# Kernel optimization log

Hardware: AMD Instinct MI355X
Metric: run time of the kernel (lower is better)

Reference implementation:

```python
import jax, jax.numpy as jnp
import numpy as np

H = 128; R = 8; VN = 100; VA = 64
N = 8192; B = 64; L = 48; E = 65536


def setup_inputs() -> dict:
    key = jax.random.key(0)
    ks = jax.random.split(key, 24)
    s = 0.05
    nodeTypes = jax.random.randint(ks[0], (N,), 0, VN)
    edge_index = jax.random.randint(ks[1], (2, E), 0, N)
    edge_attr = jax.random.randint(ks[2], (E,), 0, R)
    bs = jnp.repeat(jnp.arange(B), N // B)              # sorted node->graph map
    nodes_bs = jnp.full((B,), N // B, dtype=jnp.int32)  # nodes per graph
    len_seq = jax.random.randint(ks[3], (B,), 1, L + 1).at[0].set(L)  # max == L
    sequence_input = (jax.random.uniform(ks[4], (N, L)) < 0.05).astype(jnp.float32)
    action_input = jax.random.randint(ks[5], (B,), 0, VA)
    params = dict(
        emb_nodes=jax.random.normal(ks[6], (VN, H)) * s,
        emb_actions=jax.random.normal(ks[7], (VA, H)) * s,
        rgcn_rel=jax.random.normal(ks[8], (3, R, H, H)) * s,   # per-layer relation weights
        rgcn_root=jax.random.normal(ks[9], (3, H, H)) * s,
        rgcn_bias=jnp.zeros((3, H)),
        gru_w_ih=jax.random.normal(ks[10], (3 * H, H)) * s,
        gru_w_hh=jax.random.normal(ks[11], (3 * H, H)) * s,
        gru_b_ih=jnp.zeros((3 * H,)),
        gru_b_hh=jnp.zeros((3 * H,)),
        linA_w=jax.random.normal(ks[12], (H, H)) * s,
        linA_b=jnp.zeros((H,)),
        linAf_w=jax.random.normal(ks[13], (VA, H)) * s,
        linAf_b=jnp.zeros((VA,)),
        linN_w=jax.random.normal(ks[14], (H, 2 * H)) * s,
        linN_b=jnp.zeros((H,)),
        linNf_w=jax.random.normal(ks[15], (1, H)) * s,
        linNf_b=jnp.zeros((1,)),
    )
    return dict(nodeTypes=nodeTypes, edge_index=edge_index, edge_attr=edge_attr,
                bs=bs, nodes_bs=nodes_bs, len_seq=len_seq,
                sequence_input=sequence_input, action_input=action_input, **params)


def reference(nodeTypes, edge_index, edge_attr, bs, nodes_bs, len_seq,
              sequence_input, action_input,
              emb_nodes, emb_actions, rgcn_rel, rgcn_root, rgcn_bias,
              gru_w_ih, gru_w_hh, gru_b_ih, gru_b_hh,
              linA_w, linA_b, linAf_w, linAf_b,
              linN_w, linN_b, linNf_w, linNf_b):
    n = nodeTypes.shape[0]
    b = nodes_bs.shape[0]
    h = emb_nodes.shape[1]
    r = rgcn_rel.shape[1]
    l = sequence_input.shape[1]

    x = emb_nodes[nodeTypes]                               # [N,H]
    src, dst = edge_index[0], edge_index[1]
    seg = dst * r + edge_attr                              # per (target, relation) segment
    cnt = jax.ops.segment_sum(jnp.ones((src.shape[0],), x.dtype), seg, n * r)
    denom = jnp.maximum(cnt, 1.0).reshape(n, r, 1)
    for li in range(3):
        agg = jax.ops.segment_sum(x[src], seg, n * r).reshape(n, r, h) / denom
        x = jax.nn.relu(jnp.einsum('nrh,rho->no', agg, rgcn_rel[li])
                        + x @ rgcn_root[li] + rgcn_bias[li])

    # global mean pool -> graph embedding
    h_G = jax.ops.segment_sum(x, bs, b) / nodes_bs[:, None].astype(x.dtype)  # [B,H]
    action = jax.nn.relu(h_G @ linA_w.T + linA_b) @ linAf_w.T + linAf_b      # [B,VA]

    sos = emb_actions[action_input][:, None, :]            # [B,1,H]
    # sequence embeddings: sum over nodes in each graph of seq[i,t]*x[i]
    emb_seq = sequence_input[:, :, None] * x[:, None, :]   # [N,L,H]
    out = jax.ops.segment_sum(emb_seq, bs, b)              # [B,L,H]
    input_gru = jnp.concatenate([sos, out], axis=1)[:, :l] # packed GRU only sees first L steps

    # single-layer GRU, h0 = h_G (torch gate order r,z,n)
    xW = input_gru @ gru_w_ih.T + gru_b_ih                 # [B,L,3H]
    def step(hprev, xw):
        hW = hprev @ gru_w_hh.T + gru_b_hh
        xr, xz, xn = jnp.split(xw, 3, -1)
        hr, hz, hn = jnp.split(hW, 3, -1)
        rg = jax.nn.sigmoid(xr + hr)
        zg = jax.nn.sigmoid(xz + hz)
        ng = jnp.tanh(xn + rg * hn)
        hnew = (1.0 - zg) * ng + zg * hprev
        return hnew, hnew
    _, hs = jax.lax.scan(step, h_G, jnp.swapaxes(xW, 0, 1))
    seq_out = jnp.swapaxes(hs, 0, 1)                       # [B,L,H]
    mask = jnp.arange(l)[None, :] < len_seq[:, None]       # pad_packed zero-pads
    seq_out = seq_out * mask[:, :, None]

    out_gru = seq_out[bs]                                  # repeat_interleave -> [N,L,H]
    concats = jnp.concatenate(
        [out_gru, jnp.broadcast_to(x[:, None, :], (n, l, h))], axis=2)  # [N,L,2H]
    hid = jax.nn.relu(concats @ linN_w.T + linN_b)         # [N,L,H]
    logits = (hid @ linNf_w.T + linNf_b)[..., 0]           # [N,L]

    # scatter_softmax over nodes grouped by graph (dim 0)
    m = jax.lax.stop_gradient(jax.ops.segment_max(logits, bs, b))
    e = jnp.exp(logits - m[bs])
    ssum = jax.ops.segment_sum(e, bs, b)
    nodes_final = e / ssum[bs]
    return action, nodes_final
```

## Files before the change

### kernel.cpp

```cpp
#include <hip/hip_runtime.h>
#include <hip/hip_bf16.h>

#define H   128
#define RR  8
#define NN  8192
#define BB  64
#define LL  48
#define EE  65536
#define NPG 128
#define VA  64
#define NSEG (NN*RR)
#define GPB 16

typedef unsigned short u16;
typedef unsigned int   u32;

__device__ __forceinline__ float b2f(u16 u) {
    union { u32 i; float f; } v; v.i = ((u32)u) << 16; return v.f;
}
__device__ __forceinline__ u16 f2b(float f) {
    union { float f; u32 i; } v; v.f = f;
    u32 x = v.i;
    return (u16)((x + 0x7fffu + ((x >> 16) & 1u)) >> 16);
}
__device__ __forceinline__ float2 up2(u32 p) {
    union { u32 i; float f; } a, b;
    a.i = p << 16; b.i = p & 0xffff0000u;
    return make_float2(a.f, b.f);
}
__device__ __forceinline__ u32 pk2(float a, float b) {
    return ((u32)f2b(b) << 16) | (u32)f2b(a);
}
__device__ __forceinline__ float rcpf(float x) { return __builtin_amdgcn_rcpf(x); }
__device__ __forceinline__ u32 cvtpk(float lo, float hi) {
    u32 r;
    asm("v_cvt_pk_bf16_f32 %0, %1, %2" : "=v"(r) : "v"(lo), "v"(hi));
    return r;
}

#define K_LOG2E  1.4426950408889634f
#define K_2LOG2E 2.8853900817779268f

typedef __attribute__((ext_vector_type(8))) short bf16x8;
typedef __attribute__((ext_vector_type(4))) float f32x4;
typedef __attribute__((ext_vector_type(4))) unsigned short u16x4;

__global__ __launch_bounds__(256) void k_prep(const int* __restrict__ nodeTypes,
                                              const float* __restrict__ emb_nodes,
                                              const float* __restrict__ rel,
                                              const float* __restrict__ root,
                                              const float* __restrict__ w_ih,
                                              float* __restrict__ x0,
                                              u16* __restrict__ WTt,
                                              u16* __restrict__ WTih,
                                              float* __restrict__ hGsum,
                                              int* __restrict__ fill) {
    int idx = blockIdx.x * 256 + threadIdx.x;
    if (idx < NSEG) fill[idx] = 0;
    if (idx < 384 * H) WTih[idx] = f2b(w_ih[idx]);
    if (idx < BB * H) hGsum[idx] = 0.f;
    if (idx < NN * H) {
        int n = idx >> 7, h = idx & (H - 1);
        x0[idx] = emb_nodes[(size_t)nodeTypes[n] * H + h];
    }
    int j = idx - NN * H;
    if (j < 0 || j >= 3 * 147456) return;
    int li  = j / 147456;
    int rem = j - li * 147456;
    int tile = rem / 36864;
    int r2   = rem - tile * 36864;
    int ks   = r2 / 1024;
    int r3   = r2 - ks * 1024;
    int sub  = r3 >> 9;
    int r4   = r3 & 511;
    int lane = r4 >> 3, jj = r4 & 7;
    int col = tile * 32 + sub * 16 + (lane & 15);
    int k   = ks * 32 + (lane >> 4) * 8 + jj;
    float v;
    if (k < 1024) v = rel[(((size_t)li * RR + (k >> 7)) * H + (k & 127)) * H + col];
    else          v = root[((size_t)li * H + (k - 1024)) * H + col];
    WTt[j] = f2b(v);
}

__global__ __launch_bounds__(256) void k_hist(const int* __restrict__ edge_index,
                                              const int* __restrict__ edge_attr,
                                              int* __restrict__ fill) {
    int e = blockIdx.x * 256 + threadIdx.x;
    if (e < EE) {
        int seg = edge_index[EE + e] * RR + edge_attr[e];
        atomicAdd(&fill[seg], 1);
    }
}

__global__ __launch_bounds__(256) void k_scan1(const int* __restrict__ fill,
                                               int* __restrict__ bsum) {
    __shared__ int red[4];
    int tid = threadIdx.x, lane = tid & 63, wv = tid >> 6;
    int v = fill[blockIdx.x * 256 + tid];
#pragma unroll
    for (int off = 32; off >= 1; off >>= 1) v += __shfl_down(v, off, 64);
    if (lane == 0) red[wv] = v;
    __syncthreads();
    if (tid == 0) bsum[blockIdx.x] = red[0] + red[1] + red[2] + red[3];
}

__global__ __launch_bounds__(256) void k_scan2(const int* __restrict__ bsum,
                                               int* __restrict__ boff,
                                               int* __restrict__ rowptr) {
    __shared__ int s[256];
    int tid = threadIdx.x;
    int v0 = bsum[tid];
    s[tid] = v0;
    __syncthreads();
    for (int off = 1; off < 256; off <<= 1) {
        int v = (tid >= off) ? s[tid - off] : 0;
        __syncthreads();
        s[tid] += v;
        __syncthreads();
    }
    boff[tid] = s[tid] - v0;
    if (tid == 255) rowptr[NSEG] = s[255];
}

__global__ __launch_bounds__(256) void k_scan3(const int* __restrict__ boff,
                                               int* __restrict__ fill,
                                               int* __restrict__ rowptr) {
    __shared__ int s[256];
    int tid = threadIdx.x;
    int g = blockIdx.x * 256 + tid;
    int c = fill[g];
    s[tid] = c;
    __syncthreads();
    for (int off = 1; off < 256; off <<= 1) {
        int v = (tid >= off) ? s[tid - off] : 0;
        __syncthreads();
        s[tid] += v;
        __syncthreads();
    }
    int r = boff[blockIdx.x] + s[tid] - c;
    rowptr[g] = r;
    fill[g] = r;
}

__global__ __launch_bounds__(256) void k_scatter(const int* __restrict__ edge_index,
                                                 const int* __restrict__ edge_attr,
                                                 int* __restrict__ fill,
                                                 int* __restrict__ colidx) {
    int e = blockIdx.x * 256 + threadIdx.x;
    if (e < EE) {
        int seg = edge_index[EE + e] * RR + edge_attr[e];
        int pos = atomicAdd(&fill[seg], 1);
        colidx[pos] = edge_index[e];
    }
}

#define RGN 16
#define EPRE 512

__global__ __launch_bounds__(512) void k_rgcn(const float* __restrict__ xin,
                                              float* __restrict__ xout,
                                              const u16* __restrict__ WTt,
                                              const float* __restrict__ bias,
                                              const int* __restrict__ rowptr,
                                              const int* __restrict__ colidx,
                                              float* __restrict__ hGsum) {
    __shared__ u32 ab[RGN * 580];
    __shared__ int begs[RGN * RR + 1];
    __shared__ int eidx[EPRE];
    int tid = threadIdx.x, wv = tid >> 6, lane = tid & 63;
    int n0 = blockIdx.x * RGN, segbase = n0 * RR;

    if (tid <= RGN * RR) begs[tid] = rowptr[segbase + tid];
    __syncthreads();
    int E0 = begs[0], ne = begs[RGN * RR] - E0;
    for (int i = tid; i < ne && i < EPRE; i += 512) eidx[i] = colidx[E0 + i];
    __syncthreads();

    for (int s = wv; s < RGN * RR; s += 8) {
        int beg = begs[s], end = begs[s + 1];
        float a0 = 0.f, a1 = 0.f;
        for (int e = beg; e < end; ++e) {
            int off = e - E0;
            int src = (off < EPRE) ? eidx[off] : colidx[e];
            float2 v = ((const float2*)(xin + (size_t)src * H))[lane];
            a0 += v.x; a1 += v.y;
        }
        float inv = 1.f / fmaxf((float)(end - beg), 1.f);
        ab[(s >> 3) * 580 + ((s & 7) << 6) + lane] = pk2(a0 * inv, a1 * inv);
    }
    for (int i = wv; i < RGN; i += 8) {
        const float* xr = xin + (size_t)(n0 + i) * H + 2 * lane;
        ab[i * 580 + 512 + lane] = pk2(xr[0], xr[1]);
    }
    __syncthreads();

    int m = lane & 15, quad = lane >> 4;
    const u32* aP = ab + m * 580 + quad * 4;
    const u32* bT = (const u32*)WTt + (size_t)(wv >> 1) * 36 * 512 + (wv & 1) * 256 + lane * 4;
    f32x4 acc0 = {0.f, 0.f, 0.f, 0.f};
    bf16x8 b0c = *(const bf16x8*)bT;
    for (int ks = 0; ks < 36; ++ks) {
        bf16x8 b0n;
        if (ks < 35) b0n = *(const bf16x8*)(bT + (ks + 1) * 512);
        bf16x8 a = *(const bf16x8*)(aP + ks * 16);
        acc0 = __builtin_amdgcn_mfma_f32_16x16x32_bf16(a, b0c, acc0, 0, 0, 0);
        b0c = b0n;
    }
    int c0 = wv * 16 + m;
    float bv0 = bias[c0];
    float so0 = 0.f;
#pragma unroll
    for (int rg = 0; rg < 4; ++rg) {
        int n = n0 + quad * 4 + rg;
        float o0 = fmaxf(acc0[rg] + bv0, 0.f);
        xout[(size_t)n * H + c0] = o0;
        so0 += o0;
    }
    if (hGsum) {
        so0 += __shfl_xor(so0, 16, 64);
        so0 += __shfl_xor(so0, 32, 64);
        if (quad == 0) {
            int g = n0 >> 7;
            atomicAdd(&hGsum[g * H + c0], so0);
        }
    }
}

__global__ __launch_bounds__(256) void k_pool_seq(const float* __restrict__ hGsum,
                                                  const int* __restrict__ nodes_bs,
                                                  const float* __restrict__ linA_w,
                                                  const float* __restrict__ linA_b,
                                                  const float* __restrict__ linAf_w,
                                                  const float* __restrict__ linAf_b,
                                                  float* __restrict__ hG,
                                                  float* __restrict__ out,
                                                  const float* __restrict__ xf,
                                                  const float* __restrict__ seq,
                                                  const float* __restrict__ emb_actions,
                                                  const int* __restrict__ action_input,
                                                  float* __restrict__ igG) {
    __shared__ float xg[64][H];
    __shared__ u16 lists[LL][64];
    __shared__ int cnts[LL];
    int tid = threadIdx.x;

    if (blockIdx.x < BB) {
        float* hgs = &xg[0][0];
        float* t1  = &xg[1][0];
        int b = blockIdx.x, h = tid;
        if (h < H) {
            float hg = hGsum[(size_t)b * H + h] / (float)nodes_bs[b];
            hG[(size_t)b * H + h] = hg;
            hgs[h] = hg;
        }
        __syncthreads();
        if (h < H) {
            float acc = linA_b[h];
            const float* wr = linA_w + (size_t)h * H;
            for (int k = 0; k < H; ++k) acc += wr[k] * hgs[k];
            t1[h] = fmaxf(acc, 0.f);
        }
        __syncthreads();
        if (h < VA) {
            float a = linAf_b[h];
            const float* w2 = linAf_w + (size_t)h * H;
            for (int k = 0; k < H; ++k) a += w2[k] * t1[k];
            out[(size_t)b * VA + h] = a;
        }
        return;
    }

    int b = blockIdx.x - BB;
    int col = tid & 127, tg = tid >> 7;
    float acc[24];
#pragma unroll
    for (int m = 0; m < 24; ++m) acc[m] = 0.f;

    for (int chunk = 0; chunk < 2; ++chunk) {
        int i0 = b * NPG + chunk * 64;
        __syncthreads();
        if (tid < LL) cnts[tid] = 0;
        __syncthreads();
        for (int idx = tid; idx < 64 * H / 4; idx += 256)
            ((float4*)&xg[0][0])[idx] = ((const float4*)(xf + (size_t)i0 * H))[idx];
        for (int idx = tid; idx < 64 * LL; idx += 256) {
            int i = idx / LL, t = idx - i * LL;
            if (seq[(size_t)(i0 + i) * LL + t] != 0.f) {
                int p = atomicAdd(&cnts[t], 1);
                lists[t][p] = (u16)i;
            }
        }
        __syncthreads();
        for (int m = 0; m < 24; ++m) {
            int t = tg + 2 * m;
            int c = cnts[t];
            float a = acc[m];
            for (int p = 0; p < c; ++p) a += xg[lists[t][p]][col];
            acc[m] = a;
        }
    }
    if (tid < H)
        igG[((size_t)b * LL) * H + tid] = emb_actions[(size_t)action_input[b] * H + tid];
#pragma unroll
    for (int m = 0; m < 24; ++m) {
        int t = tg + 2 * m;
        if (t < LL - 1)
            igG[((size_t)b * LL + t + 1) * H + col] = acc[m];
    }
}

__global__ __launch_bounds__(256) void k_xw(const float* __restrict__ igG,
                                            const u16* __restrict__ WTih,
                                            const float* __restrict__ b_ih,
                                            const float* __restrict__ b_hh,
                                            u16* __restrict__ xwG) {
    __shared__ u32 ab[16 * 68];
    int tid = threadIdx.x, wv = tid >> 6, lane = tid & 63;
    int n0 = blockIdx.x * 16;
    for (int s = tid; s < 16 * 64; s += 256) {
        int row = s >> 6, kp = s & 63;
        float2 v = *(const float2*)(igG + (size_t)(n0 + row) * H + 2 * kp);
        ab[row * 68 + kp] = pk2(v.x, v.y);
    }
    __syncthreads();
    int m = lane & 15, quad = lane >> 4;
    const u32* aP = ab + m * 68 + quad * 4;
    f32x4 acc[6];
#pragma unroll
    for (int i = 0; i < 6; ++i) acc[i] = (f32x4){0.f, 0.f, 0.f, 0.f};
#pragma unroll
    for (int ks = 0; ks < 4; ++ks) {
        bf16x8 a = *(const bf16x8*)(aP + ks * 16);
#pragma unroll
        for (int tc = 0; tc < 6; ++tc) {
            int colr = wv * 96 + tc * 16 + m;
            bf16x8 bfr = *(const bf16x8*)((const u32*)WTih + (size_t)colr * 64 + quad * 4 + ks * 16);
            acc[tc] = __builtin_amdgcn_mfma_f32_16x16x32_bf16(a, bfr, acc[tc], 0, 0, 0);
        }
    }
#pragma unroll
    for (int tc = 0; tc < 6; ++tc) {
        int c = wv * 96 + tc * 16 + m;
        float bv = b_ih[c] + ((c < 256) ? b_hh[c] : 0.f);
        float sc = (c < 256) ? K_LOG2E : K_2LOG2E;
        int R = c & 127, gate = c >> 7;
#pragma unroll
        for (int rg = 0; rg < 4; ++rg) {
            int r = n0 + quad * 4 + rg;
            int bb = r / 48, tt = r - bb * 48;
            size_t o = (((((size_t)(bb >> 4) * LL + tt) * 8 + (R >> 4)) * 3 + gate) * 256)
                     + (((R >> 2) & 3) << 6) + ((bb & 15) << 2) + (R & 3);
            xwG[o] = f2b((acc[tc][rg] + bv) * sc);
        }
    }
}

#define GRU_BLKS 4
#define BX_BLKS  (NN / 32)
#define SMEM_BYTES 33024

__global__ __launch_bounds__(512) void k_gru_bx(const u16* __restrict__ xw2,
                                                const float* __restrict__ hG,
                                                const float* __restrict__ w_hh,
                                                const float* __restrict__ b_hh,
                                                const int* __restrict__ len_seq,
                                                float* __restrict__ soutG,
                                                const float* __restrict__ xf,
                                                const float* __restrict__ linN_w,
                                                const float* __restrict__ linN_b,
                                                u16* __restrict__ BxU) {
    __shared__ __align__(16) char smem[SMEM_BYTES];
    int tid = threadIdx.x;

    if (blockIdx.x >= GRU_BLKS) {
        float* xl = (float*)smem;
        float* wb = (float*)(smem + 16384);
        int bid = blockIdx.x - GRU_BLKS;
        int n0 = bid * 32;
        for (int idx = tid; idx < 32 * H; idx += 512)
            xl[idx] = xf[(size_t)n0 * H + idx];
        int col = tid & 127, g = tid >> 7;
        float bv = linN_b[col];
        float acc[8] = {bv, bv, bv, bv, bv, bv, bv, bv};
        for (int c = 0; c < 4; ++c) {
            int k0 = c * 32;
            __syncthreads();
            for (int idx = tid; idx < 32 * H; idx += 512) {
                int r = idx >> 5, kk = idx & 31;
                wb[kk * 130 + r] = linN_w[(size_t)r * (2 * H) + H + k0 + kk];
            }
            __syncthreads();
#pragma unroll
            for (int kk = 0; kk < 32; ++kk) {
                float w = wb[kk * 130 + col];
#pragma unroll
                for (int j = 0; j < 8; ++j) acc[j] += xl[(g * 8 + j) * H + k0 + kk] * w;
            }
        }
#pragma unroll
        for (int j = 0; j < 8; ++j)
            BxU[(size_t)(n0 + g * 8 + j) * H + col] = f2b(acc[j]);
        return;
    }

    u16* hA = (u16*)smem;
    int lane = tid & 63, wv = tid >> 6;
    int mi = lane & 15, quad = lane >> 4;
    int gblk = blockIdx.x;
    int g_abs = gblk * GPB + mi;
    int R0 = 16 * wv + 4 * quad;

    int eW = (((wv >> 1) * 64) + (mi + 16 * ((2 * wv + (quad >> 1)) & 3))) * 8
             + 4 * (quad & 1);

    bf16x8 wfr[3][4];
#pragma unroll
    for (int gate = 0; gate < 3; ++gate) {
        int T = wv + 8 * gate;
        float sc = (gate == 2) ? K_2LOG2E : K_LOG2E;
#pragma unroll
        for (int ks = 0; ks < 4; ++ks) {
            const float* wp = w_hh + (size_t)(16 * T + mi) * H + quad * 8 + ks * 32;
            float4 f0 = *(const float4*)wp;
            float4 f1 = *(const float4*)(wp + 4);
            bf16x8 v;
            v[0] = (short)f2b(f0.x * sc); v[1] = (short)f2b(f0.y * sc);
            v[2] = (short)f2b(f0.z * sc); v[3] = (short)f2b(f0.w * sc);
            v[4] = (short)f2b(f1.x * sc); v[5] = (short)f2b(f1.y * sc);
            v[6] = (short)f2b(f1.z * sc); v[7] = (short)f2b(f1.w * sc);
            wfr[gate][ks] = v;
        }
    }
    float4 bn = *(const float4*)(b_hh + 256 + R0);
    float4 h0 = *(const float4*)(hG + (size_t)g_abs * H + R0);
    int ls = len_seq[g_abs];

    float hp[4]  = {h0.x, h0.y, h0.z, h0.w};
    float bnn[4] = {bn.x * K_2LOG2E, bn.y * K_2LOG2E, bn.z * K_2LOG2E, bn.w * K_2LOG2E};

    auto storeh = [&](int buf, const float* hv) {
        u32 w0 = cvtpk(hv[0], hv[1]);
        u32 w1 = cvtpk(hv[2], hv[3]);
        float2 e0 = up2(w0), e1 = up2(w1);
        u32 l0 = cvtpk(hv[0] - e0.x, hv[1] - e0.y);
        u32 l1 = cvtpk(hv[2] - e1.x, hv[3] - e1.y);
        *(uint2*)&hA[buf * 4096 + eW]        = make_uint2(w0, w1);
        *(uint2*)&hA[buf * 4096 + 2048 + eW] = make_uint2(l0, l1);
    };
    auto loadxw = [&](int t, u16x4* d) {
        const u16* p = xw2 + ((((size_t)gblk * LL + t) * 8 + wv) * 3) * 256
                     + (quad << 6) + (mi << 2);
        d[0] = *(const u16x4*)(p);
        d[1] = *(const u16x4*)(p + 256);
        d[2] = *(const u16x4*)(p + 512);
    };

    auto step = [&](int t, const u16x4* x, int buf) {
        f32x4 acc[3];
        acc[0] = (f32x4){0.f, 0.f, 0.f, 0.f};
        acc[1] = (f32x4){0.f, 0.f, 0.f, 0.f};
        acc[2] = (f32x4){bnn[0], bnn[1], bnn[2], bnn[3]};
#pragma unroll
        for (int ks = 0; ks < 4; ++ks) {
            const int e = (ks * 64 + lane) * 8;
            bf16x8 bh = *(const bf16x8*)&hA[buf * 4096 + e];
            bf16x8 bl = *(const bf16x8*)&hA[buf * 4096 + 2048 + e];
#pragma unroll
            for (int gate = 0; gate < 3; ++gate) {
                acc[gate] = __builtin_amdgcn_mfma_f32_16x16x32_bf16(wfr[gate][ks], bh, acc[gate], 0, 0, 0);
                acc[gate] = __builtin_amdgcn_mfma_f32_16x16x32_bf16(wfr[gate][ks], bl, acc[gate], 0, 0, 0);
            }
        }
        float hv[4];
        float4 so;
#pragma unroll
        for (int r = 0; r < 4; ++r) {
            float xr = b2f(x[0][r]);
            float xz = b2f(x[1][r]);
            float xn = b2f(x[2][r]);
            float rg = rcpf(1.f + __builtin_amdgcn_exp2f(-(xr + acc[0][r])));
            float zg = rcpf(1.f + __builtin_amdgcn_exp2f(-(xz + acc[1][r])));
            float u  = xn + rg * acc[2][r];
            float ng = 1.f - 2.f * rcpf(__builtin_amdgcn_exp2f(u) + 1.f);
            float hn = ng + zg * (hp[r] - ng);
            hp[r] = hn;
            hv[r] = hn;
            ((float*)&so)[r] = (t < ls) ? hn : 0.f;
        }
        *(float4*)(soutG + ((size_t)g_abs * LL + t) * H + R0) = so;
        storeh(buf ^ 1, hv);
    };

    u16x4 xa[3], xb[3];
    loadxw(0, xa);
    loadxw(1, xb);
    storeh(0, hp);
    asm volatile("s_waitcnt lgkmcnt(0)\n\ts_barrier" ::: "memory");

    for (int t = 0; t < LL; t += 2) {
        step(t, xa, 0);
        if (t + 2 < LL) loadxw(t + 2, xa);
        asm volatile("s_waitcnt lgkmcnt(0)\n\ts_barrier" ::: "memory");
        step(t + 1, xb, 1);
        if (t + 3 < LL) loadxw(t + 3, xb);
        asm volatile("s_waitcnt lgkmcnt(0)\n\ts_barrier" ::: "memory");
    }
}

__global__ __launch_bounds__(256) void k_a2(const float* __restrict__ soutG,
                                            const float* __restrict__ linN_w,
                                            float* __restrict__ A2) {
    __shared__ float wb[32][130];
    __shared__ float xl[16][H];
    int tid = threadIdx.x;
    int n0 = blockIdx.x * 16;
    for (int idx = tid; idx < 16 * H; idx += 256)
        xl[idx >> 7][idx & 127] = soutG[(size_t)n0 * H + idx];
    int col = tid & 127, g = tid >> 7;
    float acc[8] = {0.f, 0.f, 0.f, 0.f, 0.f, 0.f, 0.f, 0.f};
    for (int c = 0; c < 4; ++c) {
        int k0 = c * 32;
        __syncthreads();
        for (int idx = tid; idx < 32 * H; idx += 256) {
            int r = idx >> 5, kk = idx & 31;
            wb[kk][r] = linN_w[(size_t)r * (2 * H) + k0 + kk];
        }
        __syncthreads();
#pragma unroll
        for (int kk = 0; kk < 32; ++kk) {
            float w = wb[kk][col];
#pragma unroll
            for (int j = 0; j < 8; ++j) acc[j] += xl[g * 8 + j][k0 + kk] * w;
        }
    }
#pragma unroll
    for (int j = 0; j < 8; ++j)
        A2[(size_t)(n0 + g * 8 + j) * H + col] = acc[j];
}

__global__ __launch_bounds__(256) void k_logits(const float* __restrict__ A2,
                                                const u16* __restrict__ BxU,
                                                const float* __restrict__ linNf_w,
                                                float* __restrict__ logits) {
    __shared__ float a2s[LL][130];
    __shared__ float bxs[16][130];
    __shared__ float w2s[H];
    int tid = threadIdx.x;
    int g = blockIdx.x >> 3, tile = blockIdx.x & 7;
    int n0g = g * NPG + tile * 16;

    for (int i2 = tid; i2 < LL * 64; i2 += 256) {
        int r = i2 >> 6, c2 = i2 & 63;
        *(float2*)&a2s[r][2 * c2] = *(const float2*)(A2 + ((size_t)g * LL + r) * H + 2 * c2);
    }
    for (int iu = tid; iu < 16 * 64; iu += 256) {
        int r = iu >> 6, c = iu & 63;
        float2 v = up2(((const u32*)BxU)[(size_t)(n0g + r) * 64 + c]);
        *(float2*)&bxs[r][2 * c] = v;
    }
    if (tid < H) w2s[tid] = linNf_w[tid];
    __syncthreads();

    int n = tid & 15, tt = tid >> 4;
#pragma unroll
    for (int pass = 0; pass < 3; ++pass) {
        int t = tt + 16 * pass;
        float acc = 0.f;
#pragma unroll
        for (int kp = 0; kp < 64; ++kp) {
            float2 a2 = *(const float2*)&a2s[t][2 * kp];
            float2 bx = *(const float2*)&bxs[n][2 * kp];
            float2 w  = *(const float2*)&w2s[2 * kp];
            acc += w.x * fmaxf(a2.x + bx.x, 0.f) + w.y * fmaxf(a2.y + bx.y, 0.f);
        }
        logits[(size_t)(n0g + n) * LL + t] = acc;
    }
}

__global__ __launch_bounds__(256) void k_softmax(const float* __restrict__ logits,
                                                 float* __restrict__ out) {
    __shared__ float lg[NPG][LL + 1];
    __shared__ float pm[4][LL], ps[4][LL];
    __shared__ float mv[LL], inv[LL];
    int b = blockIdx.x, tid = threadIdx.x;
    int n0 = b * NPG;
    for (int idx = tid; idx < NPG * LL; idx += 256) {
        int n = idx / LL, t = idx - n * LL;
        lg[n][t] = logits[(size_t)n0 * LL + idx];
    }
    __syncthreads();
    int t = tid & 63, seg = tid >> 6;
    if (t < LL) {
        float m = -1e30f;
        int nb = seg * 32;
        for (int n = nb; n < nb + 32; ++n) m = fmaxf(m, lg[n][t]);
        pm[seg][t] = m;
    }
    __syncthreads();
    if (tid < LL)
        mv[tid] = fmaxf(fmaxf(pm[0][tid], pm[1][tid]), fmaxf(pm[2][tid], pm[3][tid]));
    __syncthreads();
    if (t < LL) {
        float m = mv[t], s = 0.f;
        int nb = seg * 32;
        for (int n = nb; n < nb + 32; ++n) {
            float e = __expf(lg[n][t] - m);
            lg[n][t] = e;
            s += e;
        }
        ps[seg][t] = s;
    }
    __syncthreads();
    if (tid < LL)
        inv[tid] = 1.f / (ps[0][tid] + ps[1][tid] + ps[2][tid] + ps[3][tid]);
    __syncthreads();
    for (int idx = tid; idx < NPG * LL; idx += 256) {
        int n = idx / LL, tc = idx - n * LL;
        out[(size_t)BB * VA + (size_t)n0 * LL + idx] = lg[n][tc] * inv[tc];
    }
}

extern "C" void kernel_launch(void* const* d_in, const int* in_sizes, int n_in,
                              void* d_out, int out_size, void* d_ws, size_t ws_size,
                              hipStream_t stream) {
    (void)in_sizes; (void)n_in; (void)out_size; (void)ws_size;
    const int*   nodeTypes    = (const int*)d_in[0];
    const int*   edge_index   = (const int*)d_in[1];
    const int*   edge_attr    = (const int*)d_in[2];
    const int*   nodes_bs     = (const int*)d_in[4];
    const int*   len_seq      = (const int*)d_in[5];
    const float* seq_in       = (const float*)d_in[6];
    const int*   action_input = (const int*)d_in[7];
    const float* emb_nodes    = (const float*)d_in[8];
    const float* emb_actions  = (const float*)d_in[9];
    const float* rgcn_rel     = (const float*)d_in[10];
    const float* rgcn_root    = (const float*)d_in[11];
    const float* rgcn_bias    = (const float*)d_in[12];
    const float* gru_w_ih     = (const float*)d_in[13];
    const float* gru_w_hh     = (const float*)d_in[14];
    const float* gru_b_ih     = (const float*)d_in[15];
    const float* gru_b_hh     = (const float*)d_in[16];
    const float* linA_w       = (const float*)d_in[17];
    const float* linA_b       = (const float*)d_in[18];
    const float* linAf_w      = (const float*)d_in[19];
    const float* linAf_b      = (const float*)d_in[20];
    const float* linN_w       = (const float*)d_in[21];
    const float* linN_b       = (const float*)d_in[22];
    const float* linNf_w      = (const float*)d_in[23];

    char* w = (char*)d_ws;
    float* x0      = (float*)(w + 0);
    u16*   xwG     = (u16*)  (w + 0);
    float* logitsW = (float*)(w + 0);
    float* soutG   = (float*)(w + 2359296);
    float* x1      = (float*)(w + 4194304);
    float* igG     = (float*)(w + 8388608);
    float* A2      = (float*)(w + 8388608);
    u16*   BxU     = (u16*)  (w + 9961472);
    int*   bsum    = (int*)  (w + 9961472);
    int*   boff    = (int*)  (w + 9962496);
    float* hGsum   = (float*)(w + 9969664);
    int*   rowptr  = (int*)  (w + 11567104);
    int*   fill    = (int*)  (w + 11829760);
    float* hG      = (float*)(w + 12058624);
    int*   colidx  = (int*)  (w + 12091904);
    u16*   WTih    = (u16*)  (w + 12354048);
    u16*   WT      = (u16*)  (w + 12616192);

    float* out_f = (float*)d_out;

    k_prep<<<dim3(5824), dim3(256), 0, stream>>>(nodeTypes, emb_nodes, rgcn_rel,
        rgcn_root, gru_w_ih, x0, WT, WTih, hGsum, fill);
    k_hist<<<dim3(256), dim3(256), 0, stream>>>(edge_index, edge_attr, fill);
    k_scan1<<<dim3(256), dim3(256), 0, stream>>>(fill, bsum);
    k_scan2<<<dim3(1), dim3(256), 0, stream>>>(bsum, boff, rowptr);
    k_scan3<<<dim3(256), dim3(256), 0, stream>>>(boff, fill, rowptr);
    k_scatter<<<dim3(256), dim3(256), 0, stream>>>(edge_index, edge_attr, fill, colidx);

    const int rg_grid = NN / RGN;
    k_rgcn<<<dim3(rg_grid), dim3(512), 0, stream>>>(x0, x1,
        WT + 0 * 147456, rgcn_bias + 0 * H, rowptr, colidx, nullptr);
    k_rgcn<<<dim3(rg_grid), dim3(512), 0, stream>>>(x1, x0,
        WT + 1 * 147456, rgcn_bias + 1 * H, rowptr, colidx, nullptr);
    k_rgcn<<<dim3(rg_grid), dim3(512), 0, stream>>>(x0, x1,
        WT + 2 * 147456, rgcn_bias + 2 * H, rowptr, colidx, hGsum);

    k_pool_seq<<<dim3(2 * BB), dim3(256), 0, stream>>>(hGsum, nodes_bs, linA_w, linA_b,
        linAf_w, linAf_b, hG, out_f, x1, seq_in, emb_actions, action_input, igG);
    k_xw<<<dim3(BB * LL / 16), dim3(256), 0, stream>>>(igG, WTih, gru_b_ih, gru_b_hh, xwG);
    k_gru_bx<<<dim3(GRU_BLKS + BX_BLKS), dim3(512), 0, stream>>>(xwG, hG, gru_w_hh,
        gru_b_hh, len_seq, soutG, x1, linN_w, linN_b, BxU);
    k_a2<<<dim3(BB * LL / 16), dim3(256), 0, stream>>>(soutG, linN_w, A2);
    k_logits<<<dim3(BB * 8), dim3(256), 0, stream>>>(A2, BxU, linNf_w, logitsW);
    k_softmax<<<dim3(BB), dim3(256), 0, stream>>>(logitsW, out_f);
}
```

Baseline: 313.9 us.

## Merge block-offset scan into scan3 and drop bf16 low-part GRU correction

The separate single-block scan of block sums is folded into k_scan3, so every block redundantly scans the 256 block sums in shared memory and one kernel launch disappears. Separately, the GRU recurrence stops splitting the hidden state into bf16 high and low parts. It now feeds only the high bf16 part to the MFMA, halving the hidden-state LDS traffic and the MFMA count per step on the serial critical path. This lowers the precision of the recurrent matmul, and the error may build up over the 48 steps against tolerance.

```diff
diff --git a/kernel.cpp b/kernel.cpp
--- a/kernel.cpp
+++ b/kernel.cpp
@@ -104,40 +104,30 @@
     if (tid == 0) bsum[blockIdx.x] = red[0] + red[1] + red[2] + red[3];
 }
 
-__global__ __launch_bounds__(256) void k_scan2(const int* __restrict__ bsum,
-                                               int* __restrict__ boff,
-                                               int* __restrict__ rowptr) {
-    __shared__ int s[256];
-    int tid = threadIdx.x;
-    int v0 = bsum[tid];
-    s[tid] = v0;
-    __syncthreads();
-    for (int off = 1; off < 256; off <<= 1) {
-        int v = (tid >= off) ? s[tid - off] : 0;
-        __syncthreads();
-        s[tid] += v;
-        __syncthreads();
-    }
-    boff[tid] = s[tid] - v0;
-    if (tid == 255) rowptr[NSEG] = s[255];
-}
-
-__global__ __launch_bounds__(256) void k_scan3(const int* __restrict__ boff,
+__global__ __launch_bounds__(256) void k_scan3(const int* __restrict__ bsum,
                                                int* __restrict__ fill,
                                                int* __restrict__ rowptr) {
-    __shared__ int s[256];
+    __shared__ int s[256], s2[256];
+    __shared__ int boffs;
     int tid = threadIdx.x;
     int g = blockIdx.x * 256 + tid;
     int c = fill[g];
+    int b0 = bsum[tid];
     s[tid] = c;
+    s2[tid] = b0;
     __syncthreads();
     for (int off = 1; off < 256; off <<= 1) {
-        int v = (tid >= off) ? s[tid - off] : 0;
+        int v  = (tid >= off) ? s[tid - off]  : 0;
+        int v2 = (tid >= off) ? s2[tid - off] : 0;
         __syncthreads();
         s[tid] += v;
-        __syncthreads();
-    }
-    int r = boff[blockIdx.x] + s[tid] - c;
+        s2[tid] += v2;
+        __syncthreads();
+    }
+    if (blockIdx.x == 0 && tid == 255) rowptr[NSEG] = s2[255];
+    if (tid == blockIdx.x) boffs = s2[tid] - b0;
+    __syncthreads();
+    int r = boffs + s[tid] - c;
     rowptr[g] = r;
     fill[g] = r;
 }
@@ -441,11 +431,7 @@
     auto storeh = [&](int buf, const float* hv) {
         u32 w0 = cvtpk(hv[0], hv[1]);
         u32 w1 = cvtpk(hv[2], hv[3]);
-        float2 e0 = up2(w0), e1 = up2(w1);
-        u32 l0 = cvtpk(hv[0] - e0.x, hv[1] - e0.y);
-        u32 l1 = cvtpk(hv[2] - e1.x, hv[3] - e1.y);
-        *(uint2*)&hA[buf * 4096 + eW]        = make_uint2(w0, w1);
-        *(uint2*)&hA[buf * 4096 + 2048 + eW] = make_uint2(l0, l1);
+        *(uint2*)&hA[buf * 2048 + eW] = make_uint2(w0, w1);
     };
     auto loadxw = [&](int t, u16x4* d) {
         const u16* p = xw2 + ((((size_t)gblk * LL + t) * 8 + wv) * 3) * 256
@@ -463,13 +449,10 @@
 #pragma unroll
         for (int ks = 0; ks < 4; ++ks) {
             const int e = (ks * 64 + lane) * 8;
-            bf16x8 bh = *(const bf16x8*)&hA[buf * 4096 + e];
-            bf16x8 bl = *(const bf16x8*)&hA[buf * 4096 + 2048 + e];
-#pragma unroll
-            for (int gate = 0; gate < 3; ++gate) {
+            bf16x8 bh = *(const bf16x8*)&hA[buf * 2048 + e];
+#pragma unroll
+            for (int gate = 0; gate < 3; ++gate)
                 acc[gate] = __builtin_amdgcn_mfma_f32_16x16x32_bf16(wfr[gate][ks], bh, acc[gate], 0, 0, 0);
-                acc[gate] = __builtin_amdgcn_mfma_f32_16x16x32_bf16(wfr[gate][ks], bl, acc[gate], 0, 0, 0);
-            }
         }
         float hv[4];
         float4 so;
@@ -658,7 +641,6 @@
     float* A2      = (float*)(w + 8388608);
     u16*   BxU     = (u16*)  (w + 9961472);
     int*   bsum    = (int*)  (w + 9961472);
-    int*   boff    = (int*)  (w + 9962496);
     float* hGsum   = (float*)(w + 9969664);
     int*   rowptr  = (int*)  (w + 11567104);
     int*   fill    = (int*)  (w + 11829760);
@@ -673,8 +655,7 @@
         rgcn_root, gru_w_ih, x0, WT, WTih, hGsum, fill);
     k_hist<<<dim3(256), dim3(256), 0, stream>>>(edge_index, edge_attr, fill);
     k_scan1<<<dim3(256), dim3(256), 0, stream>>>(fill, bsum);
-    k_scan2<<<dim3(1), dim3(256), 0, stream>>>(bsum, boff, rowptr);
-    k_scan3<<<dim3(256), dim3(256), 0, stream>>>(boff, fill, rowptr);
+    k_scan3<<<dim3(256), dim3(256), 0, stream>>>(bsum, fill, rowptr);
     k_scatter<<<dim3(256), dim3(256), 0, stream>>>(edge_index, edge_attr, fill, colidx);
 
     const int rg_grid = NN / RGN;
```

Result: no change. 309.1 us (median of 3 runs) (-1.5%).
